# Kernel optimization log

Measured on AMD Instinct MI355X. Metric: run time of the kernel, lower is better.

## Reference

```python
import jax, jax.numpy as jnp
import numpy as np

NEG = jnp.float32(-1e30)  # finite stand-in for -inf (grad-safe)
B, T_MAX, K_MAX = 64, 2000, 400
BLANK_LOGPROB = -1.0


def setup_inputs() -> dict:
    key = jax.random.key(0)
    k1, k2, k3, k4 = jax.random.split(key, 4)
    attn = jax.random.normal(k1, (B, 1, T_MAX, K_MAX), jnp.float32)
    attn_logprob = jax.random.normal(k2, (B, 1, T_MAX, K_MAX), jnp.float32)
    in_lens = jax.random.randint(k3, (B,), K_MAX // 2, K_MAX + 1)   # text lengths in [200,400]
    out_lens = jax.random.randint(k4, (B,), T_MAX // 2, T_MAX + 1)  # mel lengths in [1000,2000]
    return {"attn": attn, "in_lens": in_lens, "out_lens": out_lens, "attn_logprob": attn_logprob}


def ctc_alignment_loss(attn_logprob, in_lens, out_lens):
    # attn_logprob: [B, 1, T, K]; targets for sample b are arange(1, in_lens[b]+1), blank=0.
    Bn, _, T, K = attn_logprob.shape
    C = K + 1
    # pad blank class (index 0) with constant blank_logprob, as in F.pad(..., value=blank_logprob)
    lp = jnp.concatenate(
        [jnp.full((Bn, T, 1), BLANK_LOGPROB, attn_logprob.dtype), attn_logprob[:, 0]], axis=-1
    )  # [B, T, C]
    # per-sample log_softmax restricted to classes [0 .. in_len] (original slices :key_len+1 first)
    cls_mask = jnp.arange(C)[None, :] <= in_lens[:, None]          # [B, C]
    lp = jnp.where(cls_mask[:, None, :], lp, NEG)
    lp = jax.nn.log_softmax(lp, axis=-1)                            # [B, T, C]

    # extended CTC state sequence: blank, 1, blank, 2, ..., K, blank  (S = 2K+1)
    S = 2 * K + 1
    s = jnp.arange(S)
    ext = jnp.where(s % 2 == 1, (s + 1) // 2, 0)                    # labels per state
    lp_ext = jnp.take(lp, ext, axis=-1)                             # [B, T, S]
    allow2 = (s % 2 == 1) & (s >= 2)                                # skip-transition allowed (targets have no repeats)

    alpha0 = jnp.full((Bn, S), NEG, lp.dtype)
    alpha0 = alpha0.at[:, 0].set(lp_ext[:, 0, 0]).at[:, 1].set(lp_ext[:, 0, 1])

    def step(alpha, inputs):
        lp_t, t = inputs  # lp_t: [B, S]
        a1 = jnp.concatenate([jnp.full((Bn, 1), NEG, alpha.dtype), alpha[:, :-1]], axis=1)
        a2 = jnp.concatenate([jnp.full((Bn, 2), NEG, alpha.dtype), alpha[:, :-2]], axis=1)
        a2 = jnp.where(allow2[None, :], a2, NEG)
        new = lp_t + jnp.logaddexp(jnp.logaddexp(alpha, a1), a2)
        alpha = jnp.where((t < out_lens)[:, None], new, alpha)      # freeze past each sample's query_len
        return alpha, None

    xs = (lp_ext.transpose(1, 0, 2)[1:], jnp.arange(1, T))
    alpha, _ = jax.lax.scan(step, alpha0, xs)

    idx_last = 2 * in_lens                                           # final blank state per sample
    a_last = jnp.take_along_axis(alpha, idx_last[:, None], axis=1)[:, 0]
    a_prev = jnp.take_along_axis(alpha, (idx_last - 1)[:, None], axis=1)[:, 0]
    ll = jnp.logaddexp(a_last, a_prev)
    # nn.CTCLoss(reduction='mean') with batch 1: divide by target length; zero_infinity -> 0
    loss = jnp.where(ll > 0.5 * NEG, -ll / in_lens.astype(lp.dtype), jnp.zeros((), lp.dtype))
    return jnp.mean(loss)


def reference(attn, in_lens, out_lens, attn_logprob):
    # attn is accepted but unused, matching the original forward signature
    return ctc_alignment_loss(attn_logprob, in_lens, out_lens)
```

## Files before the change

kernel.cpp:

```cpp
#include <hip/hip_runtime.h>
#include <cmath>


#define T_MAXN 2000
#define K_MAXN 400

typedef uint32_t uint4v __attribute__((ext_vector_type(4)));

#define G_BYTES   ((size_t)64 * T_MAXN * K_MAXN * 2)
#define LSE_OFF   G_BYTES
#define LSE_BYTES ((size_t)64 * T_MAXN * 4)
#define ZERO_OFF  (LSE_OFF + LSE_BYTES)
#define LOSS_OFF  (ZERO_OFF + 4096)
#define WS_NEED   (LOSS_OFF + 64 * 4)

__device__ __forceinline__ float dpp_wave_shr1(float x)
{
    int r = __builtin_amdgcn_update_dpp(0, (int)__float_as_uint(x),
                                        0x138 , 0xF, 0xF, true);
    return __uint_as_float((uint32_t)r);
}

template <int CTRL>
__device__ __forceinline__ float dpp_mov(float x)
{
    int r = __builtin_amdgcn_update_dpp(0, (int)__float_as_uint(x),
                                        CTRL, 0xF, 0xF, true);
    return __uint_as_float((uint32_t)r);
}

__global__ __launch_bounds__(256)
void prep_kernel(const float* __restrict__ ap_all,
                 const int* __restrict__ in_lens,
                 const int* __restrict__ out_lens,
                 float* __restrict__ lse_out,
                 _Float16* __restrict__ g_out,
                 float* __restrict__ zerobuf)
{
    const int b    = blockIdx.y;
    const int L    = in_lens[b];
    const int Tn   = out_lens[b];
    const int lane = threadIdx.x & 63;
    const int wid  = blockIdx.x * (blockDim.x >> 6) + (threadIdx.x >> 6);
    const int nw   = gridDim.x * (blockDim.x >> 6);

    if (b == 0 && wid == 0) {
        for (int i = lane; i < 1024; i += 64) zerobuf[i] = 0.0f;
    }

    const float* base = ap_all + (size_t)b * (T_MAXN * K_MAXN);
    _Float16*    gb   = g_out  + (size_t)b * (T_MAXN * K_MAXN);
    const int c0 = lane * 8;
    const int cb = (c0 < 392) ? c0 : 392;

    for (int t = wid; t < Tn; t += nw) {
        const float4* p = reinterpret_cast<const float4*>(base + (size_t)t * K_MAXN + cb);
        float4 x0 = p[0], x1 = p[1];
        float v[8] = {x0.x, x0.y, x0.z, x0.w, x1.x, x1.y, x1.z, x1.w};
        float m = -1.0f;
        #pragma unroll
        for (int j = 0; j < 8; ++j) {
            v[j] = (c0 + j < L) ? v[j] : -1e30f;
            m = fmaxf(m, v[j]);
        }
        #pragma unroll
        for (int off = 32; off; off >>= 1) m = fmaxf(m, __shfl_xor(m, off));
        float s = (lane == 0) ? __expf(-1.0f - m) : 0.0f;
        #pragma unroll
        for (int j = 0; j < 8; ++j) s += __expf(v[j] - m);
        #pragma unroll
        for (int off = 32; off; off >>= 1) s += __shfl_xor(s, off);
        if (lane == 0) lse_out[b * T_MAXN + t] = m + __logf(s);

        _Float16 h[8];
        #pragma unroll
        for (int j = 0; j < 8; ++j) h[j] = (_Float16)__expf(v[j] + 1.0f);
        if (c0 < K_MAXN)
            *reinterpret_cast<uint4v*>(gb + (size_t)t * K_MAXN + c0) =
                *reinterpret_cast<const uint4v*>(h);
    }
}

__global__ __launch_bounds__(256, 1)
void ctc_scan4w_kernel(const char* wsro,
                       const int* __restrict__ in_lens,
                       const int* __restrict__ out_lens,
                       float* loss_out)
{
    __shared__ float afin[1024];
    __shared__ float halo_sh[2][4][32];
    __shared__ float wmax_sh[2][4];

    const int b    = blockIdx.x;
    const int tid  = threadIdx.x;
    const int wid  = tid >> 6;
    const int lane = tid & 63;
    const int L    = in_lens[b];
    const int Tn   = out_lens[b];
    const uint32_t goff = (uint32_t)b * (uint32_t)(T_MAXN * K_MAXN * 2);
    const float* lse = (const float*)(wsro + LSE_OFF) + b * T_MAXN;

    const int col0 = 112 * wid - 16 + 2 * lane;
    uint32_t off, inc;
    if (col0 >= 0 && col0 < K_MAXN) { off = goff + (uint32_t)(col0 * 2) + 800u; inc = 3200u; }
    else                            { off = (uint32_t)ZERO_OFF;                 inc = 0u;    }

    float sl = 0.0f;
    if (wid == 0) {
        for (int t = lane; t < Tn; t += 64) sl += lse[t];
        #pragma unroll
        for (int o = 32; o; o >>= 1) sl += __shfl_xor(sl, o);
    }

    float a0=0.0f, a1=0.0f, a2=0.0f, a3=0.0f;
    if (wid == 0 && lane == 8) {
        a0 = 1.0f;
        a1 = (float)*reinterpret_cast<const _Float16*>(wsro + goff);
    }
    int   E  = 0;
    float t1 = 0.0f;

    #define LOADG4(QA, QB, QC, QD) do { \
        QA = *reinterpret_cast<const uint32_t*>(wsro + off); \
        QB = *reinterpret_cast<const uint32_t*>(wsro + off + 800); \
        QC = *reinterpret_cast<const uint32_t*>(wsro + off + 1600); \
        QD = *reinterpret_cast<const uint32_t*>(wsro + off + 2400); \
        off += inc; \
    } while (0)

    #define FMIXLO(DST, SRC, O) \
        asm("v_fma_mix_f32 %0, %1, %2, 0 op_sel:[0,0,0] op_sel_hi:[1,0,0]" \
            : "=v"(DST) : "v"(SRC), "v"(O))
    #define FMIXHI(DST, SRC, O) \
        asm("v_fma_mix_f32 %0, %1, %2, 0 op_sel:[1,0,0] op_sel_hi:[1,0,0]" \
            : "=v"(DST) : "v"(SRC), "v"(O))

    #define STEPF(Q) do { \
        const float e0 = a0 + t1; \
        const float e1 = a2 + a1; \
        const float o0 = a1 + e0; \
        const float o1 = a3 + e1; \
        a0 = e0; a2 = e1; \
        FMIXLO(a1, (Q), o0); \
        FMIXHI(a3, (Q), o1); \
        t1 = dpp_wave_shr1(a3); \
    } while (0)

    #define BARR do { \
        asm volatile("s_waitcnt lgkmcnt(0)" ::: "memory"); \
        __builtin_amdgcn_s_barrier(); \
        asm volatile("" ::: "memory"); \
    } while (0)

    #define EXCHANGE(PP) do { \
        float mx = fmaxf(fmaxf(a0, a1), fmaxf(a2, a3)); \
        mx = fmaxf(mx, dpp_mov<0x111>(mx)); \
        mx = fmaxf(mx, dpp_mov<0x112>(mx)); \
        mx = fmaxf(mx, dpp_mov<0x114>(mx)); \
        mx = fmaxf(mx, dpp_mov<0x118>(mx)); \
        mx = fmaxf(mx, dpp_mov<0x142>(mx)); \
        mx = fmaxf(mx, dpp_mov<0x143>(mx)); \
        if (lane == 63) wmax_sh[PP][wid] = mx; \
        if (lane >= 56) { \
            float4 bv; bv.x = a0; bv.y = a1; bv.z = a2; bv.w = a3; \
            *reinterpret_cast<float4*>(&halo_sh[PP][wid][(lane - 56) * 4]) = bv; \
        } \
        BARR; \
        float bm = fmaxf(fmaxf(wmax_sh[PP][0], wmax_sh[PP][1]), \
                         fmaxf(wmax_sh[PP][2], wmax_sh[PP][3])); \
        int e = (int)((__float_as_uint(bm) >> 23) & 0xFF) - 127; \
        E += e; \
        const float sc = __uint_as_float((uint32_t)(127 - e) << 23);   \
        if (wid > 0 && lane < 8) { \
            float4 hv = *reinterpret_cast<const float4*>(&halo_sh[PP][wid - 1][lane * 4]); \
            a0 = hv.x; a1 = hv.y; a2 = hv.z; a3 = hv.w; \
        } \
        a0 *= sc; a1 *= sc; a2 *= sc; a3 *= sc; \
        t1 = dpp_wave_shr1(a3); \
    } while (0)

    uint32_t q0,q1,q2,q3,q4,q5,q6,q7,q8,q9,q10,q11,q12,q13,q14,q15;
    LOADG4(q0,q1,q2,q3); LOADG4(q4,q5,q6,q7);
    LOADG4(q8,q9,q10,q11); LOADG4(q12,q13,q14,q15);

    int t = 1;
    int pp = 0;
    while (t + 15 < Tn) {
        STEPF(q0);  STEPF(q1);  STEPF(q2);  STEPF(q3);  LOADG4(q0,q1,q2,q3);
        STEPF(q4);  STEPF(q5);  STEPF(q6);  STEPF(q7);  LOADG4(q4,q5,q6,q7);
        STEPF(q8);  STEPF(q9);  STEPF(q10); STEPF(q11); LOADG4(q8,q9,q10,q11);
        STEPF(q12); STEPF(q13); STEPF(q14); STEPF(q15); LOADG4(q12,q13,q14,q15);
        EXCHANGE(pp);
        pp ^= 1;
        t += 16;
    }
    {
        const int r = Tn - t;
        if (r > 0)  STEPF(q0);
        if (r > 1)  STEPF(q1);
        if (r > 2)  STEPF(q2);
        if (r > 3)  STEPF(q3);
        if (r > 4)  STEPF(q4);
        if (r > 5)  STEPF(q5);
        if (r > 6)  STEPF(q6);
        if (r > 7)  STEPF(q7);
        if (r > 8)  STEPF(q8);
        if (r > 9)  STEPF(q9);
        if (r > 10) STEPF(q10);
        if (r > 11) STEPF(q11);
        if (r > 12) STEPF(q12);
        if (r > 13) STEPF(q13);
        if (r > 14) STEPF(q14);
    }

    if (lane >= 8) {
        const int gidx = 224 * wid - 32 + 4 * lane;
        afin[gidx]     = a0;
        afin[gidx + 1] = a1;
        afin[gidx + 2] = a2;
        afin[gidx + 3] = a3;
    }
    __syncthreads();
    if (tid == 0) {
        float tot = afin[2 * L] + afin[2 * L - 1];
        float lossb = 0.0f;
        if (tot > 0.0f) {
            double ll = log((double)tot)
                      + (double)E * 0.69314718055994530942
                      + (double)(-(double)Tn - (double)sl);
            lossb = (float)(-ll / (double)L);
        }
        loss_out[b] = lossb;
    }
    #undef STEPF
    #undef FMIXLO
    #undef FMIXHI
    #undef LOADG4
    #undef BARR
    #undef EXCHANGE
}

__global__ __launch_bounds__(256)
void lse_kernel(const float* __restrict__ ap_all,
                const int* __restrict__ in_lens,
                float* __restrict__ lse_out)
{
    const int lane = threadIdx.x & 63;
    const int wglob = blockIdx.x * (blockDim.x >> 6) + (threadIdx.x >> 6);
    const int nwav = gridDim.x * (blockDim.x >> 6);
    const int nrows = 64 * T_MAXN;

    for (int row = wglob; row < nrows; row += nwav) {
        const int b = row / T_MAXN;
        const int L = in_lens[b];
        const float* rp = ap_all + (size_t)row * K_MAXN;
        const int c0 = lane * 8;
        const int cb = (c0 < 392) ? c0 : 392;
        const float4* p = reinterpret_cast<const float4*>(rp + cb);
        float4 x0 = p[0], x1 = p[1];
        float v[8] = {x0.x, x0.y, x0.z, x0.w, x1.x, x1.y, x1.z, x1.w};
        float m = -1.0f;
        #pragma unroll
        for (int j = 0; j < 8; ++j) {
            v[j] = (c0 + j < L) ? v[j] : -1e30f;
            m = fmaxf(m, v[j]);
        }
        #pragma unroll
        for (int off = 32; off; off >>= 1) m = fmaxf(m, __shfl_xor(m, off));
        float s = (lane == 0) ? __expf(-1.0f - m) : 0.0f;
        #pragma unroll
        for (int j = 0; j < 8; ++j) s += __expf(v[j] - m);
        #pragma unroll
        for (int off = 32; off; off >>= 1) s += __shfl_xor(s, off);
        if (lane == 0) lse_out[row] = m + __logf(s);
    }
}

__global__ __launch_bounds__(64)
void ctc_scan_kernel(const float* __restrict__ ap_all,
                     const int* __restrict__ in_lens,
                     const int* __restrict__ out_lens,
                     const float* __restrict__ lse_all,
                     float* __restrict__ loss_out)
{
    __shared__ float afin[1024];

    const int b    = blockIdx.x;
    const int lane = threadIdx.x;
    const int L    = in_lens[b];
    const int Tn   = out_lens[b];
    const float* ap  = ap_all + (size_t)b * (T_MAXN * K_MAXN);
    const float* lse = lse_all + b * T_MAXN;

    const float LOG2E = 1.4426950408889634f;
    const int c0 = lane * 8;
    const int cb = (c0 < 392) ? c0 : 392;
    const float* rbase = ap + cb;
    float fa0,fa1,fa2,fa3,fa4,fa5,fa6,fa7;
    float fb0,fb1,fb2,fb3,fb4,fb5,fb6,fb7;
    #define MASKC(J, FA, FB) do { bool ok = (c0 + (J)) < L; \
        FA = ok ? LOG2E : 0.0f; FB = ok ? LOG2E : -1000.0f; } while (0)
    MASKC(0,fa0,fb0); MASKC(1,fa1,fb1); MASKC(2,fa2,fb2); MASKC(3,fa3,fb3);
    MASKC(4,fa4,fb4); MASKC(5,fa5,fb5); MASKC(6,fa6,fb6); MASKC(7,fa7,fb7);
    #undef MASKC

    float4 p0a,p0b,p1a,p1b,p2a,p2b,p3a,p3b;
    #define LOADROW(PA, PB, T) do { \
        const float4* _p = reinterpret_cast<const float4*>(rbase + (size_t)(T) * K_MAXN); \
        PA = _p[0]; PB = _p[1]; } while (0)
    LOADROW(p0a,p0b,1); LOADROW(p1a,p1b,2); LOADROW(p2a,p2b,3); LOADROW(p3a,p3b,4);

    float sl = 0.0f;
    for (int t = lane; t < Tn; t += 64) sl += lse[t];
    #pragma unroll
    for (int off = 32; off; off >>= 1) sl += __shfl_xor(sl, off);

    float x00 = ap[0];
    float a0=0,a1=0,a2=0,a3=0,a4=0,a5=0,a6=0,a7=0;
    float a8=0,a9=0,a10=0,a11=0,a12=0,a13=0,a14=0,a15=0;
    if (lane == 0) {
        a0 = 1.0f;
        a1 = __builtin_amdgcn_exp2f(fmaf(x00, LOG2E, LOG2E));
    }
    int E = 0;

    #define STEP(A0, A1) do { \
        float t1 = __shfl_up(a15, 1); \
        t1 = lane ? t1 : 0.0f; \
        const float f0 = __builtin_amdgcn_exp2f(fmaf((A0).x, fa0, fb0)); \
        const float f1 = __builtin_amdgcn_exp2f(fmaf((A0).y, fa1, fb1)); \
        const float f2 = __builtin_amdgcn_exp2f(fmaf((A0).z, fa2, fb2)); \
        const float f3 = __builtin_amdgcn_exp2f(fmaf((A0).w, fa3, fb3)); \
        const float f4 = __builtin_amdgcn_exp2f(fmaf((A1).x, fa4, fb4)); \
        const float f5 = __builtin_amdgcn_exp2f(fmaf((A1).y, fa5, fb5)); \
        const float f6 = __builtin_amdgcn_exp2f(fmaf((A1).z, fa6, fb6)); \
        const float f7 = __builtin_amdgcn_exp2f(fmaf((A1).w, fa7, fb7)); \
        const float e0 = a0 + t1,   e1 = a2 + a1,   e2 = a4 + a3,   e3 = a6 + a5; \
        const float e4 = a8 + a7,   e5 = a10 + a9,  e6 = a12 + a11, e7 = a14 + a13; \
        const float o0 = a1 + e0,   o1 = a3 + e1,   o2 = a5 + e2,   o3 = a7 + e3; \
        const float o4 = a9 + e4,   o5 = a11 + e5,  o6 = a13 + e6,  o7 = a15 + e7; \
        a0 = e0; a2 = e1; a4 = e2; a6 = e3; a8 = e4; a10 = e5; a12 = e6; a14 = e7; \
        a1 = f0*o0; a3 = f1*o1; a5 = f2*o2; a7 = f3*o3; \
        a9 = f4*o4; a11 = f5*o5; a13 = f6*o6; a15 = f7*o7; \
    } while (0)

    #define RESCALE do { \
        float mx = fmaxf(fmaxf(fmaxf(fmaxf(a0,a1),fmaxf(a2,a3)),fmaxf(fmaxf(a4,a5),fmaxf(a6,a7))), \
                         fmaxf(fmaxf(fmaxf(a8,a9),fmaxf(a10,a11)),fmaxf(fmaxf(a12,a13),fmaxf(a14,a15)))); \
        _Pragma("unroll") \
        for (int off = 32; off; off >>= 1) mx = fmaxf(mx, __shfl_xor(mx, off)); \
        int e = (int)((__float_as_uint(mx) >> 23) & 0xFF) - 127; \
        if (e != 0) { \
            E += e; \
            a0 = ldexpf(a0,-e);  a1 = ldexpf(a1,-e);  a2 = ldexpf(a2,-e);  a3 = ldexpf(a3,-e); \
            a4 = ldexpf(a4,-e);  a5 = ldexpf(a5,-e);  a6 = ldexpf(a6,-e);  a7 = ldexpf(a7,-e); \
            a8 = ldexpf(a8,-e);  a9 = ldexpf(a9,-e);  a10= ldexpf(a10,-e); a11= ldexpf(a11,-e); \
            a12= ldexpf(a12,-e); a13= ldexpf(a13,-e); a14= ldexpf(a14,-e); a15= ldexpf(a15,-e); \
        } \
    } while (0)

    int t = 1;
    while (t + 3 < Tn) {
        int tl;
        STEP(p0a,p0b); tl = (t+4 < T_MAXN) ? t+4 : T_MAXN-1; LOADROW(p0a,p0b,tl);
        STEP(p1a,p1b); tl = (t+5 < T_MAXN) ? t+5 : T_MAXN-1; LOADROW(p1a,p1b,tl);
        STEP(p2a,p2b); tl = (t+6 < T_MAXN) ? t+6 : T_MAXN-1; LOADROW(p2a,p2b,tl);
        STEP(p3a,p3b); tl = (t+7 < T_MAXN) ? t+7 : T_MAXN-1; LOADROW(p3a,p3b,tl);
        if ((t & 7) == 5) RESCALE;
        t += 4;
    }
    if (t < Tn) { STEP(p0a,p0b); ++t; }
    if (t < Tn) { STEP(p1a,p1b); ++t; }
    if (t < Tn) { STEP(p2a,p2b); ++t; }

    afin[16*lane+0]=a0;  afin[16*lane+1]=a1;  afin[16*lane+2]=a2;  afin[16*lane+3]=a3;
    afin[16*lane+4]=a4;  afin[16*lane+5]=a5;  afin[16*lane+6]=a6;  afin[16*lane+7]=a7;
    afin[16*lane+8]=a8;  afin[16*lane+9]=a9;  afin[16*lane+10]=a10; afin[16*lane+11]=a11;
    afin[16*lane+12]=a12; afin[16*lane+13]=a13; afin[16*lane+14]=a14; afin[16*lane+15]=a15;
    __syncthreads();
    if (lane == 0) {
        float tot = afin[2*L] + afin[2*L-1];
        float lossb = 0.0f;
        if (tot > 0.0f) {
            double ll = log((double)tot)
                      + (double)E * 0.69314718055994530942
                      + (double)(-(double)Tn - (double)sl);
            lossb = (float)(-ll / (double)L);
        }
        loss_out[b] = lossb;
    }
    #undef STEP
    #undef RESCALE
    #undef LOADROW
}

__global__ void mean_kernel(const float* __restrict__ loss, float* __restrict__ out)
{
    float v = loss[threadIdx.x];
    #pragma unroll
    for (int off = 32; off; off >>= 1) v += __shfl_xor(v, off);
    if (threadIdx.x == 0) out[0] = v * (1.0f / 64.0f);
}

extern "C" void kernel_launch(void* const* d_in, const int* in_sizes, int n_in,
                              void* d_out, int out_size, void* d_ws, size_t ws_size,
                              hipStream_t stream)
{
    const int*   in_lens  = (const int*)d_in[1];
    const int*   out_lens = (const int*)d_in[2];
    const float* ap       = (const float*)d_in[3];
    float*       out      = (float*)d_out;

    if (ws_size >= WS_NEED) {
        char*     wsb     = (char*)d_ws;
        _Float16* g       = (_Float16*)wsb;
        float*    lse_ws  = (float*)(wsb + LSE_OFF);
        float*    zb      = (float*)(wsb + ZERO_OFF);
        float*    loss_ws = (float*)(wsb + LOSS_OFF);
        hipLaunchKernelGGL(prep_kernel, dim3(32, 64), dim3(256), 0, stream,
                           ap, in_lens, out_lens, lse_ws, g, zb);
        hipLaunchKernelGGL(ctc_scan4w_kernel, dim3(64), dim3(256), 0, stream,
                           (const char*)wsb, in_lens, out_lens, loss_ws);
        hipLaunchKernelGGL(mean_kernel, dim3(1), dim3(64), 0, stream, loss_ws, out);
    } else {
        float* lse_ws  = (float*)d_ws;
        float* loss_ws = (float*)((char*)d_ws + (size_t)64 * T_MAXN * 4);
        hipLaunchKernelGGL(lse_kernel, dim3(512), dim3(256), 0, stream,
                           ap, in_lens, lse_ws);
        hipLaunchKernelGGL(ctc_scan_kernel, dim3(64), dim3(64), 0, stream,
                           ap, in_lens, out_lens, lse_ws, loss_ws);
        hipLaunchKernelGGL(mean_kernel, dim3(1), dim3(64), 0, stream, loss_ws, out);
    }
}
```

Measured before the change: 117.0 us.

## Split CTC scan across eight waves with one label per lane and skip masked loads

The per-sample CTC forward scan moves from 4 waves holding two labels per lane to 8 waves holding one label per lane. This halves the serial dependent arithmetic per time step, at the cost of more frequent cross-wave halo exchanges and barriers (every 12 steps instead of 16). Each lane also now issues one 16-bit load per step instead of four 32-bit loads per four steps. Separately, the prep kernel skips global loads for lanes whose columns lie beyond the sample's text length, cutting memory traffic for short samples.

```diff
diff --git a/kernel.cpp b/kernel.cpp
--- a/kernel.cpp
+++ b/kernel.cpp
@@ -6,6 +6,7 @@
 #define K_MAXN 400
 
 typedef uint32_t uint4v __attribute__((ext_vector_type(4)));
+typedef float    float2v __attribute__((ext_vector_type(2)));
 
 #define G_BYTES   ((size_t)64 * T_MAXN * K_MAXN * 2)
 #define LSE_OFF   G_BYTES
@@ -52,11 +53,19 @@
     _Float16*    gb   = g_out  + (size_t)b * (T_MAXN * K_MAXN);
     const int c0 = lane * 8;
     const int cb = (c0 < 392) ? c0 : 392;
+    const bool ldon = (c0 < L);
 
     for (int t = wid; t < Tn; t += nw) {
-        const float4* p = reinterpret_cast<const float4*>(base + (size_t)t * K_MAXN + cb);
-        float4 x0 = p[0], x1 = p[1];
-        float v[8] = {x0.x, x0.y, x0.z, x0.w, x1.x, x1.y, x1.z, x1.w};
+        float v[8];
+        if (ldon) {
+            const float4* p = reinterpret_cast<const float4*>(base + (size_t)t * K_MAXN + cb);
+            float4 x0 = p[0], x1 = p[1];
+            v[0]=x0.x; v[1]=x0.y; v[2]=x0.z; v[3]=x0.w;
+            v[4]=x1.x; v[5]=x1.y; v[6]=x1.z; v[7]=x1.w;
+        } else {
+            #pragma unroll
+            for (int j = 0; j < 8; ++j) v[j] = -1e30f;
+        }
         float m = -1.0f;
         #pragma unroll
         for (int j = 0; j < 8; ++j) {
@@ -81,15 +90,15 @@
     }
 }
 
-__global__ __launch_bounds__(256, 1)
-void ctc_scan4w_kernel(const char* wsro,
+__global__ __launch_bounds__(512, 1)
+void ctc_scan8w_kernel(const char* wsro,
                        const int* __restrict__ in_lens,
                        const int* __restrict__ out_lens,
                        float* loss_out)
 {
     __shared__ float afin[1024];
-    __shared__ float halo_sh[2][4][32];
-    __shared__ float wmax_sh[2][4];
+    __shared__ float halo_sh[2][8][24];
+    __shared__ float wmax_sh[2][8];
 
     const int b    = blockIdx.x;
     const int tid  = threadIdx.x;
@@ -100,10 +109,10 @@
     const uint32_t goff = (uint32_t)b * (uint32_t)(T_MAXN * K_MAXN * 2);
     const float* lse = (const float*)(wsro + LSE_OFF) + b * T_MAXN;
 
-    const int col0 = 112 * wid - 16 + 2 * lane;
+    const int col0 = 52 * wid - 12 + lane;
     uint32_t off, inc;
-    if (col0 >= 0 && col0 < K_MAXN) { off = goff + (uint32_t)(col0 * 2) + 800u; inc = 3200u; }
-    else                            { off = (uint32_t)ZERO_OFF;                 inc = 0u;    }
+    if (col0 >= 0 && col0 < K_MAXN) { off = goff + (uint32_t)(col0 * 2) + 800u; inc = 800u; }
+    else                            { off = (uint32_t)ZERO_OFF;                 inc = 0u;   }
 
     float sl = 0.0f;
     if (wid == 0) {
@@ -112,38 +121,29 @@
         for (int o = 32; o; o >>= 1) sl += __shfl_xor(sl, o);
     }
 
-    float a0=0.0f, a1=0.0f, a2=0.0f, a3=0.0f;
-    if (wid == 0 && lane == 8) {
+    float a0 = 0.0f, a1 = 0.0f;
+    if (wid == 0 && lane == 12) {
         a0 = 1.0f;
         a1 = (float)*reinterpret_cast<const _Float16*>(wsro + goff);
     }
     int   E  = 0;
-    float t1 = 0.0f;
-
-    #define LOADG4(QA, QB, QC, QD) do { \
-        QA = *reinterpret_cast<const uint32_t*>(wsro + off); \
-        QB = *reinterpret_cast<const uint32_t*>(wsro + off + 800); \
-        QC = *reinterpret_cast<const uint32_t*>(wsro + off + 1600); \
-        QD = *reinterpret_cast<const uint32_t*>(wsro + off + 2400); \
+    float t1 = dpp_wave_shr1(a1);
+
+    #define LOAD1(Q) do { \
+        Q = (uint32_t)*reinterpret_cast<const uint16_t*>(wsro + off); \
         off += inc; \
     } while (0)
 
     #define FMIXLO(DST, SRC, O) \
         asm("v_fma_mix_f32 %0, %1, %2, 0 op_sel:[0,0,0] op_sel_hi:[1,0,0]" \
             : "=v"(DST) : "v"(SRC), "v"(O))
-    #define FMIXHI(DST, SRC, O) \
-        asm("v_fma_mix_f32 %0, %1, %2, 0 op_sel:[1,0,0] op_sel_hi:[1,0,0]" \
-            : "=v"(DST) : "v"(SRC), "v"(O))
 
     #define STEPF(Q) do { \
-        const float e0 = a0 + t1; \
-        const float e1 = a2 + a1; \
-        const float o0 = a1 + e0; \
-        const float o1 = a3 + e1; \
-        a0 = e0; a2 = e1; \
-        FMIXLO(a1, (Q), o0); \
-        FMIXHI(a3, (Q), o1); \
-        t1 = dpp_wave_shr1(a3); \
+        const float e = a0 + t1; \
+        const float o = a1 + e; \
+        a0 = e; \
+        FMIXLO(a1, (Q), o); \
+        t1 = dpp_wave_shr1(a1); \
     } while (0)
 
     #define BARR do { \
@@ -153,7 +153,7 @@
     } while (0)
 
     #define EXCHANGE(PP) do { \
-        float mx = fmaxf(fmaxf(a0, a1), fmaxf(a2, a3)); \
+        float mx = fmaxf(a0, a1); \
         mx = fmaxf(mx, dpp_mov<0x111>(mx)); \
         mx = fmaxf(mx, dpp_mov<0x112>(mx)); \
         mx = fmaxf(mx, dpp_mov<0x114>(mx)); \
@@ -161,38 +161,49 @@
         mx = fmaxf(mx, dpp_mov<0x142>(mx)); \
         mx = fmaxf(mx, dpp_mov<0x143>(mx)); \
         if (lane == 63) wmax_sh[PP][wid] = mx; \
-        if (lane >= 56) { \
-            float4 bv; bv.x = a0; bv.y = a1; bv.z = a2; bv.w = a3; \
-            *reinterpret_cast<float4*>(&halo_sh[PP][wid][(lane - 56) * 4]) = bv; \
+        if (lane >= 52) { \
+            float2v bv; bv.x = a0; bv.y = a1; \
+            *reinterpret_cast<float2v*>(&halo_sh[PP][wid][(lane - 52) * 2]) = bv; \
         } \
         BARR; \
-        float bm = fmaxf(fmaxf(wmax_sh[PP][0], wmax_sh[PP][1]), \
-                         fmaxf(wmax_sh[PP][2], wmax_sh[PP][3])); \
+        float bm = fmaxf(fmaxf(fmaxf(wmax_sh[PP][0], wmax_sh[PP][1]), \
+                               fmaxf(wmax_sh[PP][2], wmax_sh[PP][3])), \
+                         fmaxf(fmaxf(wmax_sh[PP][4], wmax_sh[PP][5]), \
+                               fmaxf(wmax_sh[PP][6], wmax_sh[PP][7]))); \
         int e = (int)((__float_as_uint(bm) >> 23) & 0xFF) - 127; \
         E += e; \
         const float sc = __uint_as_float((uint32_t)(127 - e) << 23);   \
-        if (wid > 0 && lane < 8) { \
-            float4 hv = *reinterpret_cast<const float4*>(&halo_sh[PP][wid - 1][lane * 4]); \
-            a0 = hv.x; a1 = hv.y; a2 = hv.z; a3 = hv.w; \
+        if (wid > 0 && lane < 12) { \
+            float2v hv = *reinterpret_cast<const float2v*>(&halo_sh[PP][wid - 1][lane * 2]); \
+            a0 = hv.x; a1 = hv.y; \
         } \
-        a0 *= sc; a1 *= sc; a2 *= sc; a3 *= sc; \
-        t1 = dpp_wave_shr1(a3); \
-    } while (0)
-
-    uint32_t q0,q1,q2,q3,q4,q5,q6,q7,q8,q9,q10,q11,q12,q13,q14,q15;
-    LOADG4(q0,q1,q2,q3); LOADG4(q4,q5,q6,q7);
-    LOADG4(q8,q9,q10,q11); LOADG4(q12,q13,q14,q15);
+        a0 *= sc; a1 *= sc; \
+        t1 = dpp_wave_shr1(a1); \
+    } while (0)
+
+    uint32_t q0,q1,q2,q3,q4,q5,q6,q7,q8,q9,q10,q11;
+    LOAD1(q0); LOAD1(q1); LOAD1(q2);  LOAD1(q3);
+    LOAD1(q4); LOAD1(q5); LOAD1(q6);  LOAD1(q7);
+    LOAD1(q8); LOAD1(q9); LOAD1(q10); LOAD1(q11);
 
     int t = 1;
     int pp = 0;
-    while (t + 15 < Tn) {
-        STEPF(q0);  STEPF(q1);  STEPF(q2);  STEPF(q3);  LOADG4(q0,q1,q2,q3);
-        STEPF(q4);  STEPF(q5);  STEPF(q6);  STEPF(q7);  LOADG4(q4,q5,q6,q7);
-        STEPF(q8);  STEPF(q9);  STEPF(q10); STEPF(q11); LOADG4(q8,q9,q10,q11);
-        STEPF(q12); STEPF(q13); STEPF(q14); STEPF(q15); LOADG4(q12,q13,q14,q15);
+    while (t + 11 < Tn) {
+        STEPF(q0);  LOAD1(q0);
+        STEPF(q1);  LOAD1(q1);
+        STEPF(q2);  LOAD1(q2);
+        STEPF(q3);  LOAD1(q3);
+        STEPF(q4);  LOAD1(q4);
+        STEPF(q5);  LOAD1(q5);
+        STEPF(q6);  LOAD1(q6);
+        STEPF(q7);  LOAD1(q7);
+        STEPF(q8);  LOAD1(q8);
+        STEPF(q9);  LOAD1(q9);
+        STEPF(q10); LOAD1(q10);
+        STEPF(q11); LOAD1(q11);
         EXCHANGE(pp);
         pp ^= 1;
-        t += 16;
+        t += 12;
     }
     {
         const int r = Tn - t;
@@ -207,18 +218,12 @@
         if (r > 8)  STEPF(q8);
         if (r > 9)  STEPF(q9);
         if (r > 10) STEPF(q10);
-        if (r > 11) STEPF(q11);
-        if (r > 12) STEPF(q12);
-        if (r > 13) STEPF(q13);
-        if (r > 14) STEPF(q14);
-    }
-
-    if (lane >= 8) {
-        const int gidx = 224 * wid - 32 + 4 * lane;
+    }
+
+    if (lane >= 12) {
+        const int gidx = 104 * wid - 24 + 2 * lane;
         afin[gidx]     = a0;
         afin[gidx + 1] = a1;
-        afin[gidx + 2] = a2;
-        afin[gidx + 3] = a3;
     }
     __syncthreads();
     if (tid == 0) {
@@ -234,8 +239,7 @@
     }
     #undef STEPF
     #undef FMIXLO
-    #undef FMIXHI
-    #undef LOADG4
+    #undef LOAD1
     #undef BARR
     #undef EXCHANGE
 }
@@ -419,7 +423,7 @@
         float*    loss_ws = (float*)(wsb + LOSS_OFF);
         hipLaunchKernelGGL(prep_kernel, dim3(32, 64), dim3(256), 0, stream,
                            ap, in_lens, out_lens, lse_ws, g, zb);
-        hipLaunchKernelGGL(ctc_scan4w_kernel, dim3(64), dim3(256), 0, stream,
+        hipLaunchKernelGGL(ctc_scan8w_kernel, dim3(64), dim3(512), 0, stream,
                            (const char*)wsb, in_lens, out_lens, loss_ws);
         hipLaunchKernelGGL(mean_kernel, dim3(1), dim3(64), 0, stream, loss_ws, out);
     } else {
```

Result: slower. 146.4 us (+25.1%).
